# Optimization experiments

Hardware: AMD Instinct MI355X
Metric: run time of the kernel (lower is better)

## Reference

```python
import jax, jax.numpy as jnp
import numpy as np

N, D_IN, D_OUT = 4096, 1024, 1024

def setup_inputs() -> dict:
    key = jax.random.key(0)
    ks = jax.random.split(key, 7)
    s = 1.0 / np.sqrt(D_IN)
    return {
        "x": jax.random.normal(ks[0], (N, D_IN), dtype=jnp.float32),
        "W1": jax.random.normal(ks[1], (D_OUT, D_IN), dtype=jnp.float32) * s,
        "b1": jax.random.normal(ks[2], (D_OUT,), dtype=jnp.float32) * 0.01,
        "W2": jax.random.normal(ks[3], (D_OUT, D_IN), dtype=jnp.float32) * s,
        "b2": jax.random.normal(ks[4], (D_OUT,), dtype=jnp.float32) * 0.01,
        "W3": jax.random.normal(ks[5], (D_OUT, D_IN), dtype=jnp.float32) * s,
        "b3": jax.random.normal(ks[6], (D_OUT,), dtype=jnp.float32) * 0.01,
        "output_dim": D_OUT,
    }

def reference(x, W1, b1, W2, b2, W3, b3, output_dim):
    # q, k, v: [N, D_OUT]  (torch Linear: x @ W.T + b)
    q = x @ W1.T + b1
    k = x @ W2.T + b2
    v = x @ W3.T + b3
    # NOTE: original computes K @ Q^T (not Q @ K^T) — keep faithful.
    scale = 1.0 / jnp.sqrt(jnp.asarray(output_dim, dtype=x.dtype))
    attn = jax.nn.softmax(jnp.einsum("nd,md->nm", k, q) * scale, axis=-1)  # [N, N]
    # value.unsqueeze(0) * attn.unsqueeze(-1) summed over axis 1 == attn @ v
    return attn @ v  # [N, D_OUT]
```

## Files before the change

### kernel.cpp

```cpp
#include <hip/hip_runtime.h>


typedef short bf16x8 __attribute__((ext_vector_type(8)));
typedef float f32x4  __attribute__((ext_vector_type(4)));

__device__ __forceinline__ short f2bf(float f) {
    unsigned u = __builtin_bit_cast(unsigned, f);
    u += 0x7FFFu + ((u >> 16) & 1u);
    return (short)(u >> 16);
}
__device__ __forceinline__ float bf2f(short s) {
    return __builtin_bit_cast(float, (unsigned)((unsigned short)s) << 16);
}

__device__ __forceinline__ void gld_lds16(const short* g, short* l) {
    __builtin_amdgcn_global_load_lds(
        (const __attribute__((address_space(1))) void*)g,
        (__attribute__((address_space(3))) void*)l, 16, 0, 0);
}

template<int CMODE>
__global__ __launch_bounds__(512)
void gemm256(const short* __restrict__ A, int lda,
             const short* __restrict__ B, int ldb,
             const float* __restrict__ bias,
             short* __restrict__ Cout, int ldc, float scale,
             int K, size_t zstride)
{
    __shared__ __align__(16) short As[2][256 * 64];
    __shared__ __align__(16) short Bs[2][256 * 64];

    const int tid  = threadIdx.x;
    const int lane = tid & 63;
    const int wave = tid >> 6;
    const int wr   = wave >> 2;
    const int wc   = wave & 3;
    const int quad = lane >> 4;
    const int l16  = lane & 15;
    const size_t bm0 = (size_t)blockIdx.y * 256;
    const size_t bn0 = (size_t)blockIdx.x * 256;
    const int koff = blockIdx.z * K;

    f32x4 acc[8][4] = {};

    const int srow = lane >> 3;
    const int scol = ((lane & 7) ^ srow) << 3;
    const short* Ag = A + (bm0 + srow) * (size_t)lda + koff + scol;
    const short* Bg = B + (bn0 + srow) * (size_t)ldb + koff + scol;

    const int NT = K >> 6;

    auto stage = [&](int b, int k0) {
#pragma unroll
        for (int i = 0; i < 4; ++i) {
            const int j = wave * 4 + i;
            gld_lds16(Ag + (size_t)(8 * j) * lda + k0, &As[b][j * 512]);
        }
#pragma unroll
        for (int i = 0; i < 4; ++i) {
            const int j = wave * 4 + i;
            gld_lds16(Bg + (size_t)(8 * j) * ldb + k0, &Bs[b][j * 512]);
        }
    };

    stage(0, 0);
    asm volatile("s_waitcnt vmcnt(0)" ::: "memory");
    __builtin_amdgcn_s_barrier();
    __builtin_amdgcn_sched_barrier(0);

    bf16x8 af[4][2], bfr[2][2];
    int buf = 0;

    for (int t = 0; t < NT; ++t) {
        if (t + 1 < NT) stage(buf ^ 1, (t + 1) << 6);

#pragma unroll
        for (int ph = 0; ph < 4; ++ph) {
            const int Mq = ph >> 1;
            const int Nq = (ph == 1 || ph == 2) ? 1 : 0;
            if (ph == 0 || ph == 2) {
#pragma unroll
                for (int m4 = 0; m4 < 4; ++m4) {
                    const int r = wr * 128 + (Mq * 4 + m4) * 16 + l16;
                    const short* base = &As[buf][r * 64];
#pragma unroll
                    for (int ks = 0; ks < 2; ++ks)
                        af[m4][ks] = *(const bf16x8*)(
                            base + ((((ks << 2) + quad) ^ (r & 7)) << 3));
                }
            }
            if (ph != 2) {
#pragma unroll
                for (int n2 = 0; n2 < 2; ++n2) {
                    const int r = wc * 64 + (Nq * 2 + n2) * 16 + l16;
                    const short* base = &Bs[buf][r * 64];
#pragma unroll
                    for (int ks = 0; ks < 2; ++ks)
                        bfr[n2][ks] = *(const bf16x8*)(
                            base + ((((ks << 2) + quad) ^ (r & 7)) << 3));
                }
            }
            __builtin_amdgcn_s_barrier();
            __builtin_amdgcn_s_setprio(1);
#pragma unroll
            for (int ks = 0; ks < 2; ++ks)
#pragma unroll
                for (int m4 = 0; m4 < 4; ++m4)
#pragma unroll
                    for (int n2 = 0; n2 < 2; ++n2)
                        acc[Mq * 4 + m4][Nq * 2 + n2] =
                            __builtin_amdgcn_mfma_f32_16x16x32_bf16(
                                af[m4][ks], bfr[n2][ks],
                                acc[Mq * 4 + m4][Nq * 2 + n2], 0, 0, 0);
            __builtin_amdgcn_s_setprio(0);
            __builtin_amdgcn_s_barrier();
        }

        asm volatile("s_waitcnt vmcnt(0)" ::: "memory");
        __builtin_amdgcn_s_barrier();
        __builtin_amdgcn_sched_barrier(0);
        buf ^= 1;
    }

    short* Cs = Cout + ((CMODE == 3) ? (size_t)blockIdx.z * zstride : 0);
#pragma unroll
    for (int mt = 0; mt < 8; ++mt) {
#pragma unroll
        for (int nt = 0; nt < 4; ++nt) {
            const size_t col = bn0 + wc * 64 + nt * 16 + l16;
            const float bc = (CMODE == 0) ? bias[col] : 0.0f;
#pragma unroll
            for (int r = 0; r < 4; ++r) {
                const size_t row = bm0 + wr * 128 + mt * 16 + quad * 4 + r;
                float v = acc[mt][nt][r] * scale + bc;
                if (CMODE == 2) v = __expf(v);
                Cs[row * (size_t)ldc + col] = f2bf(v);
            }
        }
    }
}

__global__ __launch_bounds__(256)
void transpose_v(const short* __restrict__ qkv, short* __restrict__ vt)
{
    __shared__ short sh[64][72];
    const int n0 = blockIdx.x * 64, d0 = blockIdx.y * 64;
    const int t = threadIdx.x;
    const int r = t >> 2, c = (t & 3) << 4;

    const short* src = qkv + (size_t)(n0 + r) * 3072 + 2048 + d0 + c;
    *(int4*)(&sh[r][c])     = *(const int4*)(src);
    *(int4*)(&sh[r][c + 8]) = *(const int4*)(src + 8);
    __syncthreads();

    short tmp[16];
#pragma unroll
    for (int j = 0; j < 16; j++) tmp[j] = sh[c + j][r];
    short* dst = vt + (size_t)(d0 + r) * 4096 + n0 + c;
    *(int4*)(dst)     = *(const int4*)(tmp);
    *(int4*)(dst + 8) = *(const int4*)(tmp + 8);
}

__global__ __launch_bounds__(256)
void reduce4div(const short* __restrict__ E, const short* __restrict__ outp,
                float* __restrict__ out)
{
    const int row = blockIdx.x;
    const int t = threadIdx.x;
    const int wave = t >> 6, lane = t & 63;

    const short* e = E + (size_t)row * 4096 + (t << 4);
    short sh[16];
    *(int4*)(sh)     = *(const int4*)(e);
    *(int4*)(sh + 8) = *(const int4*)(e + 8);
    float s = 0.0f;
#pragma unroll
    for (int i = 0; i < 16; i++) s += bf2f(sh[i]);
#pragma unroll
    for (int off = 32; off; off >>= 1) s += __shfl_down(s, off);
    __shared__ float red[4];
    if (lane == 0) red[wave] = s;
    __syncthreads();
    const float inv = 1.0f / (red[0] + red[1] + red[2] + red[3]);

    const size_t base = (size_t)row * 1024 + (t << 2);
    float a[4] = {0.0f, 0.0f, 0.0f, 0.0f};
#pragma unroll
    for (int z = 0; z < 4; z++) {
        short4 p = *(const short4*)(outp + z * (size_t)4096 * 1024 + base);
        a[0] += bf2f(p.x); a[1] += bf2f(p.y);
        a[2] += bf2f(p.z); a[3] += bf2f(p.w);
    }
    float4 o;
    o.x = a[0] * inv; o.y = a[1] * inv; o.z = a[2] * inv; o.w = a[3] * inv;
    *(float4*)(out + base) = o;
}

__global__ __launch_bounds__(256)
void prep(const float* __restrict__ x, const float* __restrict__ W1,
          const float* __restrict__ W2, const float* __restrict__ W3,
          const float* __restrict__ b1, const float* __restrict__ b2,
          const float* __restrict__ b3,
          short* __restrict__ xb, short* __restrict__ Wb,
          float* __restrict__ bcat)
{
    const int i = blockIdx.x * 256 + threadIdx.x;
    const int NX = 1048576;
    const int NW = 262144;
    if (i < NX + 3 * NW) {
        const float* src; short* dst; int j;
        if (i < NX)               { src = x;  dst = xb; j = i; }
        else if (i < NX + NW)     { src = W1; dst = Wb; j = i - NX; }
        else if (i < NX + 2 * NW) { src = W2; dst = Wb + 1048576; j = i - NX - NW; }
        else                      { src = W3; dst = Wb + 2097152; j = i - NX - 2 * NW; }
        const float4 f = ((const float4*)src)[j];
        short4 o;
        o.x = f2bf(f.x); o.y = f2bf(f.y); o.z = f2bf(f.z); o.w = f2bf(f.w);
        *(short4*)(dst + (j << 2)) = o;
    } else {
        const int j = i - (NX + 3 * NW);
        if (j < 3072)
            bcat[j] = (j < 1024) ? b1[j] : (j < 2048 ? b2[j - 1024] : b3[j - 2048]);
    }
}

extern "C" void kernel_launch(void* const* d_in, const int* in_sizes, int n_in,
                              void* d_out, int out_size, void* d_ws, size_t ws_size,
                              hipStream_t stream)
{
    const float* x  = (const float*)d_in[0];
    const float* W1 = (const float*)d_in[1];
    const float* b1 = (const float*)d_in[2];
    const float* W2 = (const float*)d_in[3];
    const float* b2 = (const float*)d_in[4];
    const float* W3 = (const float*)d_in[5];
    const float* b3 = (const float*)d_in[6];
    float* out = (float*)d_out;

    const int N = 4096, D = 1024;

    char* wsb = (char*)d_ws;
    short* vt   = (short*)wsb;
    short* E    = (short*)(wsb + (size_t)8  * 1024 * 1024);
    short* xb   = (short*)(wsb + (size_t)40 * 1024 * 1024);
    short* Wb   = (short*)(wsb + (size_t)48 * 1024 * 1024);
    float* bcat = (float*)(wsb + (size_t)54 * 1024 * 1024);
    short* qkv  = (short*)(wsb + (size_t)54 * 1024 * 1024 + 16384);
    short* outp = (short*)(wsb + (size_t)40 * 1024 * 1024);

    prep<<<(1048576 + 3 * 262144 + 3072 + 255) / 256, 256, 0, stream>>>(
        x, W1, W2, W3, b1, b2, b3, xb, Wb, bcat);

    dim3 gqkv(3 * D / 256, N / 256);
    gemm256<0><<<gqkv, 512, 0, stream>>>(xb, D, Wb, D, bcat,
                                         qkv, 3 * D, 1.0f, D, 0);

    dim3 gt(N / 64, D / 64);
    transpose_v<<<gt, 256, 0, stream>>>(qkv, vt);

    dim3 gs(N / 256, N / 256);
    gemm256<2><<<gs, 512, 0, stream>>>(qkv + D, 3 * D, qkv, 3 * D,
                                       nullptr, E, N, 0.03125f, D, 0);

    dim3 go(D / 256, N / 256, 4);
    gemm256<3><<<go, 512, 0, stream>>>(E, N, vt, N, nullptr,
                                       outp, D, 1.0f, N / 4,
                                       (size_t)N * D);

    reduce4div<<<N, 256, 0, stream>>>(E, outp, out);
}
```

Baseline: 244.8 us.

## Split K tile into halves and interleave staged loads with MFMA phases

```diff
diff --git a/kernel.cpp b/kernel.cpp
--- a/kernel.cpp
+++ b/kernel.cpp
@@ -18,6 +18,8 @@
         (const __attribute__((address_space(1))) void*)g,
         (__attribute__((address_space(3))) void*)l, 16, 0, 0);
 }
+
+#define WAITV(n) asm volatile("s_waitcnt vmcnt(" #n ")" ::: "memory")
 
 template<int CMODE>
 __global__ __launch_bounds__(512)
@@ -27,8 +29,8 @@
              short* __restrict__ Cout, int ldc, float scale,
              int K, size_t zstride)
 {
-    __shared__ __align__(16) short As[2][256 * 64];
-    __shared__ __align__(16) short Bs[2][256 * 64];
+    __shared__ __align__(16) short As[2][2][256 * 32];
+    __shared__ __align__(16) short Bs[2][2][256 * 32];
 
     const int tid  = threadIdx.x;
     const int lane = tid & 63;
@@ -43,82 +45,96 @@
 
     f32x4 acc[8][4] = {};
 
-    const int srow = lane >> 3;
-    const int scol = ((lane & 7) ^ srow) << 3;
-    const short* Ag = A + (bm0 + srow) * (size_t)lda + koff + scol;
-    const short* Bg = B + (bn0 + srow) * (size_t)ldb + koff + scol;
+    const int srow  = lane >> 2;
+    const int sgran = (lane & 3) ^ ((lane >> 3) & 3);
+    const short* Ag = A + (bm0 + srow) * (size_t)lda + koff + sgran * 8;
+    const short* Bg = B + (bn0 + srow) * (size_t)ldb + koff + sgran * 8;
+
+    const int slotr = quad ^ ((l16 >> 1) & 3);
+    const int rdA = (wr * 128 + l16) * 32 + slotr * 8;
+    const int rdB = (wc * 64  + l16) * 32 + slotr * 8;
 
     const int NT = K >> 6;
 
-    auto stage = [&](int b, int k0) {
-#pragma unroll
-        for (int i = 0; i < 4; ++i) {
-            const int j = wave * 4 + i;
-            gld_lds16(Ag + (size_t)(8 * j) * lda + k0, &As[b][j * 512]);
-        }
-#pragma unroll
-        for (int i = 0; i < 4; ++i) {
-            const int j = wave * 4 + i;
-            gld_lds16(Bg + (size_t)(8 * j) * ldb + k0, &Bs[b][j * 512]);
-        }
-    };
-
-    stage(0, 0);
-    asm volatile("s_waitcnt vmcnt(0)" ::: "memory");
+    auto stA = [&](int b, int kh, int k0) {
+#pragma unroll
+        for (int i = 0; i < 2; ++i) {
+            const int j = wave * 2 + i;
+            gld_lds16(Ag + (size_t)(j * 16) * lda + k0 + kh * 32,
+                      &As[b][kh][j * 16 * 32]);
+        }
+    };
+    auto stB = [&](int b, int kh, int k0) {
+#pragma unroll
+        for (int i = 0; i < 2; ++i) {
+            const int j = wave * 2 + i;
+            gld_lds16(Bg + (size_t)(j * 16) * ldb + k0 + kh * 32,
+                      &Bs[b][kh][j * 16 * 32]);
+        }
+    };
+
+    bf16x8 af[4], bfr[4];
+
+    auto ldA = [&](int b, int ks, int mh) {
+        const short* base = &As[b][ks][rdA + mh * 64 * 32];
+#pragma unroll
+        for (int m4 = 0; m4 < 4; ++m4)
+            af[m4] = *(const bf16x8*)(base + m4 * 16 * 32);
+    };
+    auto ldB = [&](int b, int ks) {
+        const short* base = &Bs[b][ks][rdB];
+#pragma unroll
+        for (int nt = 0; nt < 4; ++nt)
+            bfr[nt] = *(const bf16x8*)(base + nt * 16 * 32);
+    };
+    auto mmac = [&](int mh) {
+        __builtin_amdgcn_s_setprio(1);
+#pragma unroll
+        for (int m4 = 0; m4 < 4; ++m4)
+#pragma unroll
+            for (int nt = 0; nt < 4; ++nt)
+                acc[mh * 4 + m4][nt] = __builtin_amdgcn_mfma_f32_16x16x32_bf16(
+                    af[m4], bfr[nt], acc[mh * 4 + m4][nt], 0, 0, 0);
+        __builtin_amdgcn_s_setprio(0);
+    };
+
+    stA(0, 0, 0); stB(0, 0, 0);
+    stA(0, 1, 0); stB(0, 1, 0);
+    WAITV(4);
     __builtin_amdgcn_s_barrier();
-    __builtin_amdgcn_sched_barrier(0);
-
-    bf16x8 af[4][2], bfr[2][2];
+
     int buf = 0;
-
     for (int t = 0; t < NT; ++t) {
-        if (t + 1 < NT) stage(buf ^ 1, (t + 1) << 6);
-
-#pragma unroll
-        for (int ph = 0; ph < 4; ++ph) {
-            const int Mq = ph >> 1;
-            const int Nq = (ph == 1 || ph == 2) ? 1 : 0;
-            if (ph == 0 || ph == 2) {
-#pragma unroll
-                for (int m4 = 0; m4 < 4; ++m4) {
-                    const int r = wr * 128 + (Mq * 4 + m4) * 16 + l16;
-                    const short* base = &As[buf][r * 64];
-#pragma unroll
-                    for (int ks = 0; ks < 2; ++ks)
-                        af[m4][ks] = *(const bf16x8*)(
-                            base + ((((ks << 2) + quad) ^ (r & 7)) << 3));
-                }
-            }
-            if (ph != 2) {
-#pragma unroll
-                for (int n2 = 0; n2 < 2; ++n2) {
-                    const int r = wc * 64 + (Nq * 2 + n2) * 16 + l16;
-                    const short* base = &Bs[buf][r * 64];
-#pragma unroll
-                    for (int ks = 0; ks < 2; ++ks)
-                        bfr[n2][ks] = *(const bf16x8*)(
-                            base + ((((ks << 2) + quad) ^ (r & 7)) << 3));
-                }
-            }
+        const int k1 = (t + 1) << 6;
+        const bool more = (t + 1) < NT;
+
+        ldA(buf, 0, 0); ldB(buf, 0);
+        if (more) stA(buf ^ 1, 0, k1);
+        __builtin_amdgcn_s_barrier();
+        mmac(0);
+        __builtin_amdgcn_s_barrier();
+
+        ldA(buf, 0, 1);
+        if (more) stB(buf ^ 1, 0, k1);
+        __builtin_amdgcn_s_barrier();
+        mmac(1);
+        if (more) { WAITV(4); } else { WAITV(0); }
+        __builtin_amdgcn_s_barrier();
+
+        ldA(buf, 1, 0); ldB(buf, 1);
+        if (more) stA(buf ^ 1, 1, k1);
+        __builtin_amdgcn_s_barrier();
+        mmac(0);
+        __builtin_amdgcn_s_barrier();
+
+        ldA(buf, 1, 1);
+        if (more) stB(buf ^ 1, 1, k1);
+        __builtin_amdgcn_s_barrier();
+        mmac(1);
+        if (more) {
+            WAITV(4);
             __builtin_amdgcn_s_barrier();
-            __builtin_amdgcn_s_setprio(1);
-#pragma unroll
-            for (int ks = 0; ks < 2; ++ks)
-#pragma unroll
-                for (int m4 = 0; m4 < 4; ++m4)
-#pragma unroll
-                    for (int n2 = 0; n2 < 2; ++n2)
-                        acc[Mq * 4 + m4][Nq * 2 + n2] =
-                            __builtin_amdgcn_mfma_f32_16x16x32_bf16(
-                                af[m4][ks], bfr[n2][ks],
-                                acc[Mq * 4 + m4][Nq * 2 + n2], 0, 0, 0);
-            __builtin_amdgcn_s_setprio(0);
-            __builtin_amdgcn_s_barrier();
-        }
-
-        asm volatile("s_waitcnt vmcnt(0)" ::: "memory");
-        __builtin_amdgcn_s_barrier();
-        __builtin_amdgcn_sched_barrier(0);
+        }
         buf ^= 1;
     }
 
```

New measurement: 220.6 us. 9.9% less time.

## Split GEMM LDS tiles into half-buffers with staggered fine-grained prefetch pipeline

Applied to the files above, without the earlier changes.

```diff
diff --git a/kernel.cpp b/kernel.cpp
--- a/kernel.cpp
+++ b/kernel.cpp
@@ -18,6 +18,9 @@
         (const __attribute__((address_space(1))) void*)g,
         (__attribute__((address_space(3))) void*)l, 16, 0, 0);
 }
+
+#define WAITV(n) asm volatile("s_waitcnt vmcnt(" #n ")" ::: "memory")
+#define BAR() __builtin_amdgcn_s_barrier()
 
 template<int CMODE>
 __global__ __launch_bounds__(512)
@@ -27,8 +30,8 @@
              short* __restrict__ Cout, int ldc, float scale,
              int K, size_t zstride)
 {
-    __shared__ __align__(16) short As[2][256 * 64];
-    __shared__ __align__(16) short Bs[2][256 * 64];
+    __shared__ __align__(16) short As[2][2][128 * 64];
+    __shared__ __align__(16) short Bs[2][2][128 * 64];
 
     const int tid  = threadIdx.x;
     const int lane = tid & 63;
@@ -43,95 +46,125 @@
 
     f32x4 acc[8][4] = {};
 
-    const int srow = lane >> 3;
-    const int scol = ((lane & 7) ^ srow) << 3;
-    const short* Ag = A + (bm0 + srow) * (size_t)lda + koff + scol;
-    const short* Bg = B + (bn0 + srow) * (size_t)ldb + koff + scol;
+    const int srow  = lane >> 3;
+    const int sgran = (lane & 7) ^ srow;
+    const short* Ag0 = A + (bm0 + wave * 16 + srow) * (size_t)lda + koff + sgran * 8;
+    const short* Ag1 = Ag0 + (size_t)128 * lda;
+    const short* Bg0 = B + (bn0 + wave * 16 + srow) * (size_t)ldb + koff + sgran * 8;
+    const short* Bg1 = Bg0 + (size_t)128 * ldb;
+
+    const int s0  = ((quad ^ (l16 & 7)) << 3);
+    const int s1  = (((4 + quad) ^ (l16 & 7)) << 3);
+    const int rdA0 = (wr * 64 + l16) * 64;
+    const int rdB0 = (wc * 32 + l16) * 64;
 
     const int NT = K >> 6;
 
-    auto stage = [&](int b, int k0) {
-#pragma unroll
-        for (int i = 0; i < 4; ++i) {
-            const int j = wave * 4 + i;
-            gld_lds16(Ag + (size_t)(8 * j) * lda + k0, &As[b][j * 512]);
-        }
-#pragma unroll
-        for (int i = 0; i < 4; ++i) {
-            const int j = wave * 4 + i;
-            gld_lds16(Bg + (size_t)(8 * j) * ldb + k0, &Bs[b][j * 512]);
+    auto stage = [&](short* half, const short* g, int ld, int kt) {
+#pragma unroll
+        for (int i = 0; i < 2; ++i)
+            gld_lds16(g + (size_t)(i * 8) * ld + kt,
+                      half + (wave * 16 + i * 8) * 64);
+    };
+
+    bf16x8 af[4][2], bfr0[2][2], bfr1[2][2];
+
+    auto ldAf = [&](const short* Ah) {
+#pragma unroll
+        for (int m4 = 0; m4 < 4; ++m4) {
+            af[m4][0] = *(const bf16x8*)(Ah + rdA0 + m4 * 1024 + s0);
+            af[m4][1] = *(const bf16x8*)(Ah + rdA0 + m4 * 1024 + s1);
         }
     };
-
-    stage(0, 0);
-    asm volatile("s_waitcnt vmcnt(0)" ::: "memory");
-    __builtin_amdgcn_s_barrier();
+    auto ldBf = [&](bf16x8 (&bx)[2][2], const short* Bh) {
+#pragma unroll
+        for (int n2 = 0; n2 < 2; ++n2) {
+            bx[n2][0] = *(const bf16x8*)(Bh + rdB0 + n2 * 1024 + s0);
+            bx[n2][1] = *(const bf16x8*)(Bh + rdB0 + n2 * 1024 + s1);
+        }
+    };
+    auto mm = [&](int mq, int nq, bf16x8 (&bx)[2][2]) {
+        __builtin_amdgcn_s_setprio(1);
+#pragma unroll
+        for (int ks = 0; ks < 2; ++ks)
+#pragma unroll
+            for (int m4 = 0; m4 < 4; ++m4)
+#pragma unroll
+                for (int n2 = 0; n2 < 2; ++n2)
+                    acc[mq * 4 + m4][nq * 2 + n2] =
+                        __builtin_amdgcn_mfma_f32_16x16x32_bf16(
+                            af[m4][ks], bx[n2][ks],
+                            acc[mq * 4 + m4][nq * 2 + n2], 0, 0, 0);
+        __builtin_amdgcn_s_setprio(0);
+    };
+
+    stage(&As[0][0][0], Ag0, lda, 0);
+    stage(&As[0][1][0], Ag1, lda, 0);
+    stage(&Bs[0][0][0], Bg0, ldb, 0);
+    stage(&Bs[0][1][0], Bg1, ldb, 0);
+    stage(&As[1][0][0], Ag0, lda, 64);
+    stage(&Bs[1][1][0], Bg1, ldb, 64);
+    WAITV(4);
+    BAR();
     __builtin_amdgcn_sched_barrier(0);
 
-    bf16x8 af[4][2], bfr[2][2];
-    int buf = 0;
-
-    for (int t = 0; t < NT; ++t) {
-        if (t + 1 < NT) stage(buf ^ 1, (t + 1) << 6);
-
-#pragma unroll
-        for (int ph = 0; ph < 4; ++ph) {
-            const int Mq = ph >> 1;
-            const int Nq = (ph == 1 || ph == 2) ? 1 : 0;
-            if (ph == 0 || ph == 2) {
-#pragma unroll
-                for (int m4 = 0; m4 < 4; ++m4) {
-                    const int r = wr * 128 + (Mq * 4 + m4) * 16 + l16;
-                    const short* base = &As[buf][r * 64];
-#pragma unroll
-                    for (int ks = 0; ks < 2; ++ks)
-                        af[m4][ks] = *(const bf16x8*)(
-                            base + ((((ks << 2) + quad) ^ (r & 7)) << 3));
-                }
-            }
-            if (ph != 2) {
-#pragma unroll
-                for (int n2 = 0; n2 < 2; ++n2) {
-                    const int r = wc * 64 + (Nq * 2 + n2) * 16 + l16;
-                    const short* base = &Bs[buf][r * 64];
-#pragma unroll
-                    for (int ks = 0; ks < 2; ++ks)
-                        bfr[n2][ks] = *(const bf16x8*)(
-                            base + ((((ks << 2) + quad) ^ (r & 7)) << 3));
-                }
-            }
-            __builtin_amdgcn_s_barrier();
-            __builtin_amdgcn_s_setprio(1);
-#pragma unroll
-            for (int ks = 0; ks < 2; ++ks)
-#pragma unroll
-                for (int m4 = 0; m4 < 4; ++m4)
-#pragma unroll
-                    for (int n2 = 0; n2 < 2; ++n2)
-                        acc[Mq * 4 + m4][Nq * 2 + n2] =
-                            __builtin_amdgcn_mfma_f32_16x16x32_bf16(
-                                af[m4][ks], bfr[n2][ks],
-                                acc[Mq * 4 + m4][Nq * 2 + n2], 0, 0, 0);
-            __builtin_amdgcn_s_setprio(0);
-            __builtin_amdgcn_s_barrier();
+    for (int it = 0; it < NT / 2; ++it) {
+        const int k1 = it * 128 + 64;
+        const int k2 = it * 128 + 128;
+        const int k3 = it * 128 + 192;
+        const bool m2 = k2 < K, m3 = k3 < K;
+
+        ldAf(&As[0][0][0]);
+        ldBf(bfr0, &Bs[0][0][0]);
+        stage(&As[1][1][0], Ag1, lda, k1);
+        BAR();
+        mm(0, 0, bfr0);
+        ldBf(bfr1, &Bs[0][1][0]);
+        stage(&Bs[1][0][0], Bg0, ldb, k1);
+        BAR();
+        mm(0, 1, bfr1);
+        ldAf(&As[0][1][0]);
+        if (m2) stage(&As[0][0][0], Ag0, lda, k2);
+        BAR();
+        mm(1, 1, bfr1);
+        if (m2) stage(&Bs[0][1][0], Bg1, ldb, k2);
+        mm(1, 0, bfr0);
+        if (m2) { WAITV(4); } else { WAITV(0); }
+        BAR();
+
+        ldAf(&As[1][0][0]);
+        ldBf(bfr0, &Bs[1][0][0]);
+        if (m2) stage(&As[0][1][0], Ag1, lda, k2);
+        BAR();
+        mm(0, 0, bfr0);
+        ldBf(bfr1, &Bs[1][1][0]);
+        if (m2) stage(&Bs[0][0][0], Bg0, ldb, k2);
+        BAR();
+        mm(0, 1, bfr1);
+        ldAf(&As[1][1][0]);
+        if (m3) stage(&As[1][0][0], Ag0, lda, k3);
+        BAR();
+        mm(1, 1, bfr1);
+        if (m3) stage(&Bs[1][1][0], Bg1, ldb, k3);
+        mm(1, 0, bfr0);
+        if (m2) {
+            WAITV(4);
+            BAR();
         }
-
-        asm volatile("s_waitcnt vmcnt(0)" ::: "memory");
-        __builtin_amdgcn_s_barrier();
-        __builtin_amdgcn_sched_barrier(0);
-        buf ^= 1;
     }
 
     short* Cs = Cout + ((CMODE == 3) ? (size_t)blockIdx.z * zstride : 0);
 #pragma unroll
     for (int mt = 0; mt < 8; ++mt) {
+        const int mq = mt >> 2, m4 = mt & 3;
 #pragma unroll
         for (int nt = 0; nt < 4; ++nt) {
-            const size_t col = bn0 + wc * 64 + nt * 16 + l16;
+            const int nq = nt >> 1, n2 = nt & 1;
+            const size_t col = bn0 + nq * 128 + wc * 32 + n2 * 16 + l16;
             const float bc = (CMODE == 0) ? bias[col] : 0.0f;
 #pragma unroll
             for (int r = 0; r < 4; ++r) {
-                const size_t row = bm0 + wr * 128 + mt * 16 + quad * 4 + r;
+                const size_t row = bm0 + mq * 128 + wr * 64 + m4 * 16 + quad * 4 + r;
                 float v = acc[mt][nt][r] * scale + bc;
                 if (CMODE == 2) v = __expf(v);
                 Cs[row * (size_t)ldc + col] = f2bf(v);
```

After: 219.2 us. 10.5% less time.

## Shrink GEMM tiles to 128x256x32 with 2-deep prefetch and higher occupancy

Applied to the files above, without the earlier changes.

```diff
diff --git a/kernel.cpp b/kernel.cpp
--- a/kernel.cpp
+++ b/kernel.cpp
@@ -19,16 +19,20 @@
         (__attribute__((address_space(3))) void*)l, 16, 0, 0);
 }
 
+#define WAITV(n) asm volatile("s_waitcnt vmcnt(" #n ")" ::: "memory")
+#define LGKM0()  asm volatile("s_waitcnt lgkmcnt(0)" ::: "memory")
+#define BAR()    __builtin_amdgcn_s_barrier()
+
 template<int CMODE>
-__global__ __launch_bounds__(512)
-void gemm256(const short* __restrict__ A, int lda,
+__global__ __launch_bounds__(512, 4)
+void gemm128(const short* __restrict__ A, int lda,
              const short* __restrict__ B, int ldb,
              const float* __restrict__ bias,
              short* __restrict__ Cout, int ldc, float scale,
              int K, size_t zstride)
 {
-    __shared__ __align__(16) short As[2][256 * 64];
-    __shared__ __align__(16) short Bs[2][256 * 64];
+    __shared__ __align__(16) short As[2][128 * 32];
+    __shared__ __align__(16) short Bs[2][256 * 32];
 
     const int tid  = threadIdx.x;
     const int lane = tid & 63;
@@ -37,102 +41,82 @@
     const int wc   = wave & 3;
     const int quad = lane >> 4;
     const int l16  = lane & 15;
-    const size_t bm0 = (size_t)blockIdx.y * 256;
+    const size_t bm0 = (size_t)blockIdx.y * 128;
     const size_t bn0 = (size_t)blockIdx.x * 256;
     const int koff = blockIdx.z * K;
 
-    f32x4 acc[8][4] = {};
-
-    const int srow = lane >> 3;
-    const int scol = ((lane & 7) ^ srow) << 3;
-    const short* Ag = A + (bm0 + srow) * (size_t)lda + koff + scol;
-    const short* Bg = B + (bn0 + srow) * (size_t)ldb + koff + scol;
-
-    const int NT = K >> 6;
-
-    auto stage = [&](int b, int k0) {
-#pragma unroll
-        for (int i = 0; i < 4; ++i) {
-            const int j = wave * 4 + i;
-            gld_lds16(Ag + (size_t)(8 * j) * lda + k0, &As[b][j * 512]);
-        }
-#pragma unroll
-        for (int i = 0; i < 4; ++i) {
-            const int j = wave * 4 + i;
-            gld_lds16(Bg + (size_t)(8 * j) * ldb + k0, &Bs[b][j * 512]);
-        }
+    f32x4 acc[4][4] = {};
+
+    const int srow  = lane >> 2;
+    const int sgran = (lane & 3) ^ ((lane >> 3) & 3);
+    const short* Ag = A + (bm0 + wave * 16 + srow) * (size_t)lda + koff + sgran * 8;
+    const short* Bg = B + (bn0 + srow) * (size_t)ldb + koff + sgran * 8;
+
+    const int sl   = (l16 >> 1) & 3;
+    const int rdA0 = (wr * 64 + l16) * 32;
+    const int rdB0 = (wc * 64 + l16) * 32;
+    const int soff = ((quad ^ sl) << 3);
+
+    auto stage = [&](int p, int kt) {
+        gld_lds16(Ag + kt, &As[p][wave * 512]);
+#pragma unroll
+        for (int i = 0; i < 2; ++i)
+            gld_lds16(Bg + (size_t)((wave * 2 + i) * 16) * ldb + kt,
+                      &Bs[p][(wave * 2 + i) * 512]);
     };
 
+    bf16x8 af[4], bfr[4];
+    auto ldfrags = [&](int p) {
+#pragma unroll
+        for (int n = 0; n < 4; ++n)
+            bfr[n] = *(const bf16x8*)(&Bs[p][rdB0 + n * 512 + soff]);
+#pragma unroll
+        for (int m = 0; m < 4; ++m)
+            af[m] = *(const bf16x8*)(&As[p][rdA0 + m * 512 + soff]);
+    };
+    auto mm = [&]() {
+        __builtin_amdgcn_s_setprio(1);
+#pragma unroll
+        for (int m = 0; m < 4; ++m)
+#pragma unroll
+            for (int n = 0; n < 4; ++n)
+                acc[m][n] = __builtin_amdgcn_mfma_f32_16x16x32_bf16(
+                    af[m], bfr[n], acc[m][n], 0, 0, 0);
+        __builtin_amdgcn_s_setprio(0);
+    };
+
+    const int NT = K >> 5;
+
     stage(0, 0);
-    asm volatile("s_waitcnt vmcnt(0)" ::: "memory");
-    __builtin_amdgcn_s_barrier();
+    stage(1, 32);
+    WAITV(3);
+    BAR();
     __builtin_amdgcn_sched_barrier(0);
 
-    bf16x8 af[4][2], bfr[2][2];
-    int buf = 0;
-
+    int p = 0;
     for (int t = 0; t < NT; ++t) {
-        if (t + 1 < NT) stage(buf ^ 1, (t + 1) << 6);
-
-#pragma unroll
-        for (int ph = 0; ph < 4; ++ph) {
-            const int Mq = ph >> 1;
-            const int Nq = (ph == 1 || ph == 2) ? 1 : 0;
-            if (ph == 0 || ph == 2) {
-#pragma unroll
-                for (int m4 = 0; m4 < 4; ++m4) {
-                    const int r = wr * 128 + (Mq * 4 + m4) * 16 + l16;
-                    const short* base = &As[buf][r * 64];
-#pragma unroll
-                    for (int ks = 0; ks < 2; ++ks)
-                        af[m4][ks] = *(const bf16x8*)(
-                            base + ((((ks << 2) + quad) ^ (r & 7)) << 3));
-                }
-            }
-            if (ph != 2) {
-#pragma unroll
-                for (int n2 = 0; n2 < 2; ++n2) {
-                    const int r = wc * 64 + (Nq * 2 + n2) * 16 + l16;
-                    const short* base = &Bs[buf][r * 64];
-#pragma unroll
-                    for (int ks = 0; ks < 2; ++ks)
-                        bfr[n2][ks] = *(const bf16x8*)(
-                            base + ((((ks << 2) + quad) ^ (r & 7)) << 3));
-                }
-            }
-            __builtin_amdgcn_s_barrier();
-            __builtin_amdgcn_s_setprio(1);
-#pragma unroll
-            for (int ks = 0; ks < 2; ++ks)
-#pragma unroll
-                for (int m4 = 0; m4 < 4; ++m4)
-#pragma unroll
-                    for (int n2 = 0; n2 < 2; ++n2)
-                        acc[Mq * 4 + m4][Nq * 2 + n2] =
-                            __builtin_amdgcn_mfma_f32_16x16x32_bf16(
-                                af[m4][ks], bfr[n2][ks],
-                                acc[Mq * 4 + m4][Nq * 2 + n2], 0, 0, 0);
-            __builtin_amdgcn_s_setprio(0);
-            __builtin_amdgcn_s_barrier();
-        }
-
-        asm volatile("s_waitcnt vmcnt(0)" ::: "memory");
-        __builtin_amdgcn_s_barrier();
+        ldfrags(p);
+        LGKM0();
+        BAR();
+        if (t + 2 < NT) stage(p, (t + 2) << 5);
+        mm();
+        if (t + 2 < NT) { WAITV(3); } else { WAITV(0); }
         __builtin_amdgcn_sched_barrier(0);
-        buf ^= 1;
+        BAR();
+        p ^= 1;
     }
 
     short* Cs = Cout + ((CMODE == 3) ? (size_t)blockIdx.z * zstride : 0);
 #pragma unroll
-    for (int mt = 0; mt < 8; ++mt) {
-#pragma unroll
-        for (int nt = 0; nt < 4; ++nt) {
-            const size_t col = bn0 + wc * 64 + nt * 16 + l16;
+    for (int m = 0; m < 4; ++m) {
+#pragma unroll
+        for (int n = 0; n < 4; ++n) {
+            const size_t col = bn0 + wc * 64 + n * 16 + l16;
             const float bc = (CMODE == 0) ? bias[col] : 0.0f;
 #pragma unroll
             for (int r = 0; r < 4; ++r) {
-                const size_t row = bm0 + wr * 128 + mt * 16 + quad * 4 + r;
-                float v = acc[mt][nt][r] * scale + bc;
+                const size_t row = bm0 + wr * 64 + m * 16 + quad * 4 + r;
+                float v = acc[m][n][r] * scale + bc;
                 if (CMODE == 2) v = __expf(v);
                 Cs[row * (size_t)ldc + col] = f2bf(v);
             }
@@ -251,19 +235,19 @@
     prep<<<(1048576 + 3 * 262144 + 3072 + 255) / 256, 256, 0, stream>>>(
         x, W1, W2, W3, b1, b2, b3, xb, Wb, bcat);
 
-    dim3 gqkv(3 * D / 256, N / 256);
-    gemm256<0><<<gqkv, 512, 0, stream>>>(xb, D, Wb, D, bcat,
+    dim3 gqkv(3 * D / 256, N / 128);
+    gemm128<0><<<gqkv, 512, 0, stream>>>(xb, D, Wb, D, bcat,
                                          qkv, 3 * D, 1.0f, D, 0);
 
     dim3 gt(N / 64, D / 64);
     transpose_v<<<gt, 256, 0, stream>>>(qkv, vt);
 
-    dim3 gs(N / 256, N / 256);
-    gemm256<2><<<gs, 512, 0, stream>>>(qkv + D, 3 * D, qkv, 3 * D,
+    dim3 gs(N / 256, N / 128);
+    gemm128<2><<<gs, 512, 0, stream>>>(qkv + D, 3 * D, qkv, 3 * D,
                                        nullptr, E, N, 0.03125f, D, 0);
 
-    dim3 go(D / 256, N / 256, 4);
-    gemm256<3><<<go, 512, 0, stream>>>(E, N, vt, N, nullptr,
+    dim3 go(D / 256, N / 128, 4);
+    gemm128<3><<<go, 512, 0, stream>>>(E, N, vt, N, nullptr,
                                        outp, D, 1.0f, N / 4,
                                        (size_t)N * D);
 
```

New measurement: 221.2 us. 9.7% less time.
